# Kernel tuning notes

Measured on AMD Instinct MI355X. Metric: run time of the kernel, lower is better.

Reference implementation:

```python
import jax, jax.numpy as jnp
import numpy as np

PATCH = 7
STRIDE = 1
ALPHA = 0.05


def extract_patches(im, p=PATCH, s=STRIDE):
    # im: (b, c, h, w) -> (b, n_patches, c*p*p)
    pat = jax.lax.conv_general_dilated_patches(im, (p, p), (s, s), 'VALID')  # (b, c*p*p, H', W')
    b, d = pat.shape[0], pat.shape[1]
    return pat.reshape(b, d, -1).transpose(0, 2, 1)


def _coherence_l2(xp, yp):
    # xp: (Ni, d) input patches, yp: (Nt, d) target patches, both fp16
    d = xp.shape[-1]
    x2 = jnp.sum(xp * xp, axis=-1)                     # (Ni,)
    y2 = jnp.sum(yp * yp, axis=-1)                     # (Nt,)
    cross = jnp.einsum('td,id->ti', yp, xp)            # (Nt, Ni)
    dist = (y2[:, None] + x2[None, :] - 2.0 * cross) / d
    # normalize each target row by its NN distance (+alpha), then min over targets
    dist = dist / (jnp.min(dist, axis=1, keepdims=True) + jnp.asarray(ALPHA, dist.dtype))
    return jnp.min(dist, axis=0).mean()


def setup_inputs() -> dict:
    key = jax.random.key(0)
    k1, k2 = jax.random.split(key)
    x = jax.random.normal(k1, (2, 3, 96, 96), dtype=jnp.float32)
    y = jax.random.normal(k2, (2, 3, 96, 96), dtype=jnp.float32)
    return {"x": x, "y": y}


def reference(x, y):
    x16 = x.astype(jnp.float16)
    y16 = y.astype(jnp.float16)
    xp = extract_patches(x16)   # (b, N, d)
    yp = extract_patches(y16)   # (b, N, d)
    per_image = jax.vmap(_coherence_l2)(xp, yp)  # (b,)
    return per_image.mean()
```

## Files before the change

kernel.cpp:

```cpp
#include <hip/hip_runtime.h>
#include <hip/hip_fp16.h>

#define IMGS 2
#define OW 90
#define NP 8100
#define HW 96
#define CH_STRIDE 9216
#define IMG_STRIDE 27648
#define KP 192
#define MP 8192
#define ALPHA 0.05f
#define INV_D (1.0f/147.0f)
#define PAD_SENTINEL 60000.0f

typedef _Float16 half8 __attribute__((ext_vector_type(8)));
typedef float floatx4 __attribute__((ext_vector_type(4)));

#define GLD_LDS16(gp, lp)                                                     \
    __builtin_amdgcn_global_load_lds(                                         \
        (const __attribute__((address_space(1))) void*)(gp),                  \
        (__attribute__((address_space(3))) void*)(lp), 16, 0, 0)

#define XP_OFF   0
#define YP_OFF   (XP_OFF + IMGS*MP*KP*2)
#define RMIN_OFF (YP_OFF + IMGS*MP*KP*2)
#define CMIN_OFF (RMIN_OFF + IMGS*MP*4)
#define ACC_OFF  (CMIN_OFF + IMGS*MP*4)
#define CNT_OFF  (ACC_OFF + 4)

__global__ __launch_bounds__(256) void k_build(const float* __restrict__ x,
                                               const float* __restrict__ y,
                                               char* __restrict__ wsb) {
    int tid = threadIdx.x;
    int hwv = tid >> 5;
    int l = tid & 31;
    int grow = blockIdx.x * 8 + hwv;
    int tensor = grow >> 14;
    int img = (grow >> 13) & 1;
    int row = grow & (MP - 1);
    const float* src = (tensor ? y : x) + img * IMG_STRIDE;
    int py = row / OW, px = row - py * OW;
    bool rvalid = row < NP;

    float vals[8];
#pragma unroll
    for (int j = 0; j < 8; j++) {
        int k = l * 8 + j;
        float v = 0.0f;
        if (rvalid && k < 147) {
            int c = k / 49;
            int rm = k - c * 49;
            int dy = rm / 7, dx = rm - dy * 7;
            v = src[c * CH_STRIDE + (py + dy) * HW + px + dx];
        }
        vals[j] = (float)(_Float16)v;
    }
    float ss16 = 0.0f;
#pragma unroll
    for (int j = 0; j < 8; j++) ss16 = fmaf(vals[j], vals[j], ss16);
#pragma unroll
    for (int m = 1; m < 32; m <<= 1) ss16 += __shfl_xor(ss16, m, 32);

    half8 h;
#pragma unroll
    for (int j = 0; j < 8; j++) {
        float f = vals[j];
        if (tensor) f *= -2.0f;
        h[j] = (_Float16)f;
    }
    if (l == 18) {
        if (tensor) {
            h[3] = (_Float16)1.0f;
            h[4] = rvalid ? (_Float16)ss16 : (_Float16)0.0f;
        } else {
            h[3] = rvalid ? (_Float16)ss16 : (_Float16)PAD_SENTINEL;
            h[4] = rvalid ? (_Float16)1.0f : (_Float16)0.0f;
        }
    }
    if (l < 24) {
        _Float16* dst = (_Float16*)(wsb + (tensor ? YP_OFF : XP_OFF)) +
                        ((size_t)img * MP + row) * KP + l * 8;
        *(half8*)dst = h;
    }
    if (tid < 8) {
        int gi = blockIdx.x * 8 + tid;
        if (gi < IMGS * MP)
            ((int*)(wsb + RMIN_OFF))[gi] = 0x7f800000;
        else
            ((int*)(wsb + CMIN_OFF))[gi - IMGS * MP] = 0x7f800000;
    }
    if (blockIdx.x == 0 && tid == 0) {
        *(float*)(wsb + ACC_OFF) = 0.0f;
        *(int*)(wsb + CNT_OFF) = 0;
    }
}

#define R2OFF 8192

#define STAGE64(mat, buf)                                                      \
    {                                                                          \
        int rb_ = w * 16;                                                      \
        _Pragma("unroll") for (int g_ = 0; g_ < 4; g_++) {                     \
            int r_ = rb_ + g_ * 4 + (lane >> 4);                               \
            int gc_ = (lane & 15) ^ (r_ & 7);                                  \
            GLD_LDS16((mat) + (size_t)r_ * KP + gc_ * 8,                       \
                      (buf) + (rb_ + g_ * 4) * 128);                           \
        }                                                                      \
        int r2_ = rb_ + (lane >> 2);                                           \
        int gc2_ = (lane & 3) ^ ((r2_ >> 1) & 3);                              \
        GLD_LDS16((mat) + (size_t)r2_ * KP + 128 + gc2_ * 8,                   \
                  (buf) + R2OFF + rb_ * 32);                                   \
    }

#define READFRAG(buf, row, ks)                                                 \
    ((ks) < 4 ? *(const half8*)(&(buf)[(row) * 128 +                           \
                                       ((((ks) * 4 + quad) ^ ((row) & 7)) * 8)]) \
              : *(const half8*)(&(buf)[R2OFF + (row) * 32 +                    \
                                       ((quad ^ (((row) >> 1) & 3)) * 8)]))

template <int PASS>
__global__ __launch_bounds__(256, 3) void k_gemm(char* __restrict__ wsb) {
    __shared__ __align__(16) _Float16 Buf[2][10240];
    __shared__ __align__(16) int RMl[1024];
    int tid = threadIdx.x;
    int lane = tid & 63, w = tid >> 6;
    int quad = lane >> 4, col16 = lane & 15;
    int q = blockIdx.x;
    int rtile = blockIdx.y;
    int img = blockIdx.z;

    const _Float16* Res = (const _Float16*)(wsb + (PASS == 1 ? YP_OFF : XP_OFF)) +
                          ((size_t)img * MP + rtile * 128) * KP;
    const _Float16* Str = (const _Float16*)(wsb + (PASS == 1 ? XP_OFF : YP_OFF)) +
                          (size_t)img * MP * KP;

    STAGE64(Res, Buf[0]);
    STAGE64(Res + (size_t)64 * KP, Buf[1]);
    if (PASS == 2 && w == 0) {
        const char* RMg = wsb + RMIN_OFF + ((size_t)img * MP + q * 1024) * 4;
#pragma unroll
        for (int g = 0; g < 4; g++)
            GLD_LDS16(RMg + g * 1024 + lane * 16, &RMl[g * 256]);
    }
    __syncthreads();
    half8 rf[4][5];
    const _Float16* rb = Buf[w >> 1];
#pragma unroll
    for (int i = 0; i < 4; i++)
#pragma unroll
        for (int c = 0; c < 5; c++)
            rf[i][c] = READFRAG(rb, i * 16 + col16, c);
    __syncthreads();
    STAGE64(Str + (size_t)(q * 16) * 64 * KP, Buf[0]);

    float mn[4];
#pragma unroll
    for (int i = 0; i < 4; i++) mn[i] = 1e30f;
    int s0 = (w & 1) * 32;

    for (int s = 0; s < 16; s++) {
        __syncthreads();
        if (s < 15)
            STAGE64(Str + (size_t)(q * 16 + s + 1) * 64 * KP, Buf[(s + 1) & 1]);
        const _Float16* sb = Buf[s & 1];

        _Float16 rp0 = (_Float16)1.0f, rp1 = (_Float16)1.0f;
        bool pad0 = false, pad1 = false;
        if (PASS == 2) {
            int b0 = RMl[s * 64 + s0 + col16];
            int b1 = RMl[s * 64 + s0 + 16 + col16];
            pad0 = (b0 == 0x7f800000);
            pad1 = (b1 == 0x7f800000);
            rp0 = (_Float16)(INV_D / (__int_as_float(b0) * INV_D + ALPHA));
            rp1 = (_Float16)(INV_D / (__int_as_float(b1) * INV_D + ALPHA));
        }

        floatx4 acc[8];
#pragma unroll
        for (int i = 0; i < 8; i++) acc[i] = (floatx4){0.f, 0.f, 0.f, 0.f};
#pragma unroll
        for (int ks = 0; ks < 5; ks++) {
            half8 sf0 = READFRAG(sb, s0 + col16, ks);
            half8 sf1 = READFRAG(sb, s0 + 16 + col16, ks);
            if (PASS == 2) {
                half8 v0 = {rp0, rp0, rp0, rp0, rp0, rp0, rp0, rp0};
                half8 v1 = {rp1, rp1, rp1, rp1, rp1, rp1, rp1, rp1};
                sf0 = sf0 * v0;
                sf1 = sf1 * v1;
                if (ks == 4 && quad == 2) {
                    if (pad0) sf0[4] = (_Float16)PAD_SENTINEL;
                    if (pad1) sf1[4] = (_Float16)PAD_SENTINEL;
                }
            }
#pragma unroll
            for (int i = 0; i < 4; i++) {
                acc[i] = __builtin_amdgcn_mfma_f32_16x16x32_f16(
                    sf0, rf[i][ks], acc[i], 0, 0, 0);
                acc[4 + i] = __builtin_amdgcn_mfma_f32_16x16x32_f16(
                    sf1, rf[i][ks], acc[4 + i], 0, 0, 0);
            }
        }
#pragma unroll
        for (int i = 0; i < 4; i++) {
            float a = fminf(fminf(acc[i][0], acc[i][1]),
                            fminf(acc[i][2], acc[i][3]));
            float b = fminf(fminf(acc[4 + i][0], acc[4 + i][1]),
                            fminf(acc[4 + i][2], acc[4 + i][3]));
            mn[i] = fminf(mn[i], fminf(a, b));
        }
    }

    int* dst = (int*)(wsb + (PASS == 1 ? RMIN_OFF : CMIN_OFF)) + img * MP;
#pragma unroll
    for (int i = 0; i < 4; i++) {
        float best = mn[i];
        best = fminf(best, __shfl_xor(best, 16, 64));
        best = fminf(best, __shfl_xor(best, 32, 64));
        int cg = rtile * 128 + (w >> 1) * 64 + i * 16 + col16;
        if (quad == 0 && cg < NP)
            atomicMin(dst + cg, __float_as_int(best));
    }
}

__global__ __launch_bounds__(256) void k_final(char* __restrict__ wsb,
                                               float* __restrict__ out) {
    __shared__ float red[4];
    int tid = threadIdx.x;
    int gid = blockIdx.x * 256 + tid;
    const int* cm = (const int*)(wsb + CMIN_OFF);
    float s = 0.0f;
    if (gid < NP)
        s = __int_as_float(cm[gid]) + __int_as_float(cm[MP + gid]);
#pragma unroll
    for (int m = 1; m < 64; m <<= 1) s += __shfl_xor(s, m, 64);
    if ((tid & 63) == 0) red[tid >> 6] = s;
    __syncthreads();
    if (tid == 0) {
        float bs = red[0] + red[1] + red[2] + red[3];
        float* acc = (float*)(wsb + ACC_OFF);
        int* cnt = (int*)(wsb + CNT_OFF);
        atomicAdd(acc, bs);
        __threadfence();
        if (atomicAdd(cnt, 1) == 31) {
            float total = atomicAdd(acc, 0.0f);
            out[0] = total * (0.5f / NP);
        }
    }
}

extern "C" void kernel_launch(void* const* d_in, const int* in_sizes, int n_in,
                              void* d_out, int out_size, void* d_ws, size_t ws_size,
                              hipStream_t stream) {
    const float* x = (const float*)d_in[0];
    const float* y = (const float*)d_in[1];
    char* wsb = (char*)d_ws;
    float* out = (float*)d_out;

    k_build<<<4096, 256, 0, stream>>>(x, y, wsb);
    k_gemm<1><<<dim3(8, 64, IMGS), 256, 0, stream>>>(wsb);
    k_gemm<2><<<dim3(8, 64, IMGS), 256, 0, stream>>>(wsb);
    k_final<<<32, 256, 0, stream>>>(wsb, out);
}
```

Before: 164.7 us.

## Stage image rows in LDS for patch build; prefetch row minima from global

The patch-building kernel now loads each 7-row image strip into shared memory once per output row. It computes patch norms there and writes all 90 patch rows from LDS, so the old one-warp-per-patch global gather goes away. Separate blocks write the padding rows and initialise the min buffers, and the launch drops from 4096 blocks to 364. In the second GEMM pass, the per-column row-min values are read straight from global memory into registers one step ahead, replacing the LDS staging buffer. This trades redundant global loads for less parallelism in the build kernel and a little less shared memory in the GEMM.

```diff
diff --git a/kernel.cpp b/kernel.cpp
--- a/kernel.cpp
+++ b/kernel.cpp
@@ -31,67 +31,83 @@
 __global__ __launch_bounds__(256) void k_build(const float* __restrict__ x,
                                                const float* __restrict__ y,
                                                char* __restrict__ wsb) {
+    __shared__ float I[2016];
+    __shared__ float nrm[90];
     int tid = threadIdx.x;
-    int hwv = tid >> 5;
-    int l = tid & 31;
-    int grow = blockIdx.x * 8 + hwv;
-    int tensor = grow >> 14;
-    int img = (grow >> 13) & 1;
-    int row = grow & (MP - 1);
-    const float* src = (tensor ? y : x) + img * IMG_STRIDE;
-    int py = row / OW, px = row - py * OW;
-    bool rvalid = row < NP;
-
-    float vals[8];
-#pragma unroll
-    for (int j = 0; j < 8; j++) {
-        int k = l * 8 + j;
-        float v = 0.0f;
-        if (rvalid && k < 147) {
-            int c = k / 49;
-            int rm = k - c * 49;
-            int dy = rm / 7, dx = rm - dy * 7;
-            v = src[c * CH_STRIDE + (py + dy) * HW + px + dx];
-        }
-        vals[j] = (float)(_Float16)v;
-    }
-    float ss16 = 0.0f;
-#pragma unroll
-    for (int j = 0; j < 8; j++) ss16 = fmaf(vals[j], vals[j], ss16);
-#pragma unroll
-    for (int m = 1; m < 32; m <<= 1) ss16 += __shfl_xor(ss16, m, 32);
-
-    half8 h;
-#pragma unroll
-    for (int j = 0; j < 8; j++) {
-        float f = vals[j];
-        if (tensor) f *= -2.0f;
-        h[j] = (_Float16)f;
-    }
-    if (l == 18) {
-        if (tensor) {
-            h[3] = (_Float16)1.0f;
-            h[4] = rvalid ? (_Float16)ss16 : (_Float16)0.0f;
-        } else {
-            h[3] = rvalid ? (_Float16)ss16 : (_Float16)PAD_SENTINEL;
-            h[4] = rvalid ? (_Float16)1.0f : (_Float16)0.0f;
-        }
-    }
-    if (l < 24) {
-        _Float16* dst = (_Float16*)(wsb + (tensor ? YP_OFF : XP_OFF)) +
-                        ((size_t)img * MP + row) * KP + l * 8;
-        *(half8*)dst = h;
-    }
-    if (tid < 8) {
-        int gi = blockIdx.x * 8 + tid;
-        if (gi < IMGS * MP)
-            ((int*)(wsb + RMIN_OFF))[gi] = 0x7f800000;
-        else
-            ((int*)(wsb + CMIN_OFF))[gi - IMGS * MP] = 0x7f800000;
-    }
-    if (blockIdx.x == 0 && tid == 0) {
-        *(float*)(wsb + ACC_OFF) = 0.0f;
-        *(int*)(wsb + CNT_OFF) = 0;
+    int b = blockIdx.x;
+    if (b < 360) {
+        int tensor = b / 180;
+        int img = (b / 90) % 2;
+        int py = b % 90;
+        const float* src = (tensor ? y : x) + img * IMG_STRIDE;
+        for (int idx = tid; idx < 2016; idx += 256) {
+            int c = idx / 672, rem = idx % 672;
+            int dy = rem / 96, u = rem % 96;
+            I[idx] = src[c * CH_STRIDE + (py + dy) * HW + u];
+        }
+        __syncthreads();
+        if (tid < 90) {
+            float s = 0.0f;
+            for (int c = 0; c < 3; c++)
+#pragma unroll
+                for (int dy = 0; dy < 7; dy++) {
+                    const float* rowp = &I[c * 672 + dy * 96 + tid];
+#pragma unroll
+                    for (int dx = 0; dx < 7; dx++) {
+                        float v = (float)(_Float16)rowp[dx];
+                        s = fmaf(v, v, s);
+                    }
+                }
+            nrm[tid] = s;
+        }
+        __syncthreads();
+        _Float16* dstbase = (_Float16*)(wsb + (tensor ? YP_OFF : XP_OFF)) +
+                            ((size_t)img * MP + (size_t)py * 90) * KP;
+        for (int ch = tid; ch < 2160; ch += 256) {
+            int px = ch / 24, chunk = ch % 24;
+            half8 h;
+#pragma unroll
+            for (int j = 0; j < 8; j++) {
+                int k = chunk * 8 + j;
+                float f = 0.0f;
+                if (k < 147) {
+                    int c = k / 49, rm = k - c * 49;
+                    int dy = rm / 7, dx = rm - dy * 7;
+                    float v = (float)(_Float16)I[c * 672 + dy * 96 + px + dx];
+                    f = tensor ? -2.0f * v : v;
+                }
+                h[j] = (_Float16)f;
+            }
+            if (chunk == 18) {
+                float ss = nrm[px];
+                if (tensor) { h[3] = (_Float16)1.0f; h[4] = (_Float16)ss; }
+                else        { h[3] = (_Float16)ss;   h[4] = (_Float16)1.0f; }
+            }
+            *(half8*)(dstbase + (size_t)px * KP + chunk * 8) = h;
+        }
+    } else {
+        int bi = b - 360;
+        int tensor = bi >> 1, img = bi & 1;
+        _Float16* dstbase = (_Float16*)(wsb + (tensor ? YP_OFF : XP_OFF)) +
+                            (size_t)img * MP * KP;
+        for (int ch = tid; ch < (MP - NP) * 24; ch += 256) {
+            int row = NP + ch / 24, chunk = ch % 24;
+            half8 h;
+#pragma unroll
+            for (int j = 0; j < 8; j++) h[j] = (_Float16)0.0f;
+            if (chunk == 18) {
+                if (tensor) h[3] = (_Float16)1.0f;
+                else        h[3] = (_Float16)PAD_SENTINEL;
+            }
+            *(half8*)(dstbase + (size_t)row * KP + chunk * 8) = h;
+        }
+        int* mins = (int*)(wsb + RMIN_OFF);
+        for (int gi = bi * 8192 + tid; gi < bi * 8192 + 8192; gi += 256)
+            mins[gi] = 0x7f800000;
+        if (bi == 0 && tid == 0) {
+            *(float*)(wsb + ACC_OFF) = 0.0f;
+            *(int*)(wsb + CNT_OFF) = 0;
+        }
     }
 }
 
@@ -121,7 +137,6 @@
 template <int PASS>
 __global__ __launch_bounds__(256, 3) void k_gemm(char* __restrict__ wsb) {
     __shared__ __align__(16) _Float16 Buf[2][10240];
-    __shared__ __align__(16) int RMl[1024];
     int tid = threadIdx.x;
     int lane = tid & 63, w = tid >> 6;
     int quad = lane >> 4, col16 = lane & 15;
@@ -133,15 +148,10 @@
                           ((size_t)img * MP + rtile * 128) * KP;
     const _Float16* Str = (const _Float16*)(wsb + (PASS == 1 ? XP_OFF : YP_OFF)) +
                           (size_t)img * MP * KP;
+    const int* RM = (const int*)(wsb + RMIN_OFF) + img * MP;
 
     STAGE64(Res, Buf[0]);
     STAGE64(Res + (size_t)64 * KP, Buf[1]);
-    if (PASS == 2 && w == 0) {
-        const char* RMg = wsb + RMIN_OFF + ((size_t)img * MP + q * 1024) * 4;
-#pragma unroll
-        for (int g = 0; g < 4; g++)
-            GLD_LDS16(RMg + g * 1024 + lane * 16, &RMl[g * 256]);
-    }
     __syncthreads();
     half8 rf[4][5];
     const _Float16* rb = Buf[w >> 1];
@@ -158,21 +168,30 @@
     for (int i = 0; i < 4; i++) mn[i] = 1e30f;
     int s0 = (w & 1) * 32;
 
+    int cb0 = 0, cb1 = 0;
+    if (PASS == 2) {
+        cb0 = RM[(q * 16) * 64 + s0 + col16];
+        cb1 = RM[(q * 16) * 64 + s0 + 16 + col16];
+    }
+
     for (int s = 0; s < 16; s++) {
         __syncthreads();
         if (s < 15)
             STAGE64(Str + (size_t)(q * 16 + s + 1) * 64 * KP, Buf[(s + 1) & 1]);
+        int nb0 = 0, nb1 = 0;
+        if (PASS == 2 && s < 15) {
+            nb0 = RM[(q * 16 + s + 1) * 64 + s0 + col16];
+            nb1 = RM[(q * 16 + s + 1) * 64 + s0 + 16 + col16];
+        }
         const _Float16* sb = Buf[s & 1];
 
         _Float16 rp0 = (_Float16)1.0f, rp1 = (_Float16)1.0f;
         bool pad0 = false, pad1 = false;
         if (PASS == 2) {
-            int b0 = RMl[s * 64 + s0 + col16];
-            int b1 = RMl[s * 64 + s0 + 16 + col16];
-            pad0 = (b0 == 0x7f800000);
-            pad1 = (b1 == 0x7f800000);
-            rp0 = (_Float16)(INV_D / (__int_as_float(b0) * INV_D + ALPHA));
-            rp1 = (_Float16)(INV_D / (__int_as_float(b1) * INV_D + ALPHA));
+            pad0 = (cb0 == 0x7f800000);
+            pad1 = (cb1 == 0x7f800000);
+            rp0 = (_Float16)(INV_D / (__int_as_float(cb0) * INV_D + ALPHA));
+            rp1 = (_Float16)(INV_D / (__int_as_float(cb1) * INV_D + ALPHA));
         }
 
         floatx4 acc[8];
@@ -204,10 +223,11 @@
         for (int i = 0; i < 4; i++) {
             float a = fminf(fminf(acc[i][0], acc[i][1]),
                             fminf(acc[i][2], acc[i][3]));
-            float b = fminf(fminf(acc[4 + i][0], acc[4 + i][1]),
-                            fminf(acc[4 + i][2], acc[4 + i][3]));
-            mn[i] = fminf(mn[i], fminf(a, b));
-        }
+            float bmin = fminf(fminf(acc[4 + i][0], acc[4 + i][1]),
+                               fminf(acc[4 + i][2], acc[4 + i][3]));
+            mn[i] = fminf(mn[i], fminf(a, bmin));
+        }
+        if (PASS == 2 && s < 15) { cb0 = nb0; cb1 = nb1; }
     }
 
     int* dst = (int*)(wsb + (PASS == 1 ? RMIN_OFF : CMIN_OFF)) + img * MP;
@@ -256,7 +276,7 @@
     char* wsb = (char*)d_ws;
     float* out = (float*)d_out;
 
-    k_build<<<4096, 256, 0, stream>>>(x, y, wsb);
+    k_build<<<364, 256, 0, stream>>>(x, y, wsb);
     k_gemm<1><<<dim3(8, 64, IMGS), 256, 0, stream>>>(wsb);
     k_gemm<2><<<dim3(8, 64, IMGS), 256, 0, stream>>>(wsb);
     k_final<<<32, 256, 0, stream>>>(wsb, out);
```

Result: faster. 156.1 us (-5.2%).
